# Optimization experiments

Measured on AMD Instinct MI355X. Metric: run time of the kernel, lower is better.

## Reference

```python
import jax, jax.numpy as jnp
from jax import lax
import numpy as np

IMG_W = 384; IMG_H = 384; FEAT = 24; RF = 16
RATIOS = (0.5, 1.0, 2.0); SCALES = (8.0, 16.0, 32.0)
K = 9                      # len(RATIOS) * len(SCALES)
N = FEAT * FEAT * K        # 5184 anchors/proposals
MID = 24; CIN = 512
NMS_THRESH = 0.7; MIN_SIZE = 16.0


def _make_anchors():
    # Faithful port of RPN._get_anchors (vectorized over the grid).
    area = float(RF * RF)
    base = []
    for r in RATIOS:
        cols = np.round(np.sqrt(area / r)); rows = np.round(cols * r)
        x0 = 0.5 * RF - 0.5 * (cols - 1); x1 = 0.5 * RF + 0.5 * (cols - 1)
        y0 = 0.5 * RF - 0.5 * (rows - 1); y1 = 0.5 * RF + 0.5 * (rows - 1)
        aw = x1 - x0 + 1; ah = y1 - y0 + 1
        acx = x0 + 0.5 * (aw - 1); acy = y0 + 0.5 * (ah - 1)
        for s in SCALES:
            nx0 = acx - 0.5 * (aw * s - 1.0); nx1 = acx + 0.5 * (aw * s - 1.0)
            ny0 = acy - 0.5 * (ah * s - 1.0); ny1 = acy + 0.5 * (ah * s - 1.0)
            w = nx1 - nx0 + 1; h = ny1 - ny0 + 1
            base.append([nx0 + 0.5 * (w - 1), ny0 + 0.5 * (h - 1), w, h])
    base = np.asarray(base, np.float32)  # (K,4) as (cx, cy, w, h)
    ii, jj = np.meshgrid(np.arange(FEAT), np.arange(FEAT), indexing='ij')
    g = np.broadcast_to(base, (FEAT, FEAT, K, 4)).copy()  # (H, W, K, 4)
    g[..., 0] += (jj * RF)[:, :, None]
    g[..., 1] += (ii * RF)[:, :, None]
    a = g.reshape(-1, 4)  # matches permute(1,2,0).reshape(-1,4) ordering
    ax0 = a[:, 0] - 0.5 * (a[:, 2] - 1.0); ay0 = a[:, 1] - 0.5 * (a[:, 3] - 1.0)
    ax1 = a[:, 2] + ax0 - 1.0; ay1 = a[:, 3] + ay0 - 1.0
    valid = (ax0 >= 0) & (ay0 >= 0) & (ax1 < IMG_W) & (ay1 < IMG_H)
    return jnp.asarray(a, jnp.float32), jnp.asarray(valid)


def setup_inputs() -> dict:
    key = jax.random.key(0)
    ks = jax.random.split(key, 6)
    anchors, valid_mask = _make_anchors()
    return {
        'x': jax.random.normal(ks[0], (1, CIN, FEAT, FEAT), jnp.float32),
        'labels_class': jax.random.randint(ks[1], (N,), 0, 21, jnp.int32),
        'W_rpn': jax.random.normal(ks[2], (MID, CIN, 3, 3), jnp.float32) * 0.02,
        'b_rpn': jnp.zeros((MID,), jnp.float32),
        'W_cls': jax.random.normal(ks[3], (2 * K, MID), jnp.float32) * 0.05,
        'b_cls': jnp.zeros((2 * K,), jnp.float32),
        'W_reg': jax.random.normal(ks[4], (4 * K, MID), jnp.float32) * 0.01,
        'b_reg': jnp.zeros((4 * K,), jnp.float32),
        'anchors': anchors,
        'valid_mask': valid_mask,
    }


def _forward(x, W_rpn, b_rpn, W_cls, b_cls, W_reg, b_reg, anchors, valid_mask, labels_class):
    # 3x3 conv + relu, then 1x1 cls/reg heads
    h = jax.nn.relu(
        lax.conv_general_dilated(x, W_rpn, (1, 1), ((1, 1), (1, 1)),
                                 dimension_numbers=('NCHW', 'OIHW', 'NCHW'))
        + b_rpn[None, :, None, None])
    cls_out = (jnp.einsum('nchw,oc->nohw', h, W_cls) + b_cls[None, :, None, None])[0]
    cls_out = cls_out.transpose(1, 2, 0).reshape(-1, 2)   # [N,2]
    reg_out = (jnp.einsum('nchw,oc->nohw', h, W_reg) + b_reg[None, :, None, None])[0]
    reg_out = reg_out.transpose(1, 2, 0).reshape(-1, 4)   # [N,4]

    # anchors -> proposals (cx, cy, w, h); computed for all anchors, validity masked below
    ax, ay, aw, ah = anchors[:, 0], anchors[:, 1], anchors[:, 2], anchors[:, 3]
    tx, ty, tw, th = reg_out[:, 0], reg_out[:, 1], reg_out[:, 2], reg_out[:, 3]
    px = ax + aw * tx; py = ay + ah * ty
    pw = aw * jnp.exp(tw); ph = ah * jnp.exp(th)
    proposals = jnp.stack((px, py, pw, ph), axis=1)

    # offset2bbox + clip_boxes
    x0 = px - 0.5 * (pw - 1.0); y0 = py - 0.5 * (ph - 1.0)
    x1 = pw + x0 - 1.0; y1 = ph + y0 - 1.0
    x0 = jnp.clip(x0, 0.0, IMG_W - 1.0); x1 = jnp.clip(x1, 0.0, IMG_W - 1.0)
    y0 = jnp.clip(y0, 0.0, IMG_H - 1.0); y1 = jnp.clip(y1, 0.0, IMG_H - 1.0)
    ws = x1 - x0 + 1.0; hs = y1 - y0 + 1.0

    probs = jax.nn.softmax(cls_out, axis=1)[:, 1]
    validity = valid_mask & (ws >= MIN_SIZE) & (hs >= MIN_SIZE)

    # greedy NMS (padded/masked: invalid boxes get score -1 and are never kept)
    scores = jnp.where(validity, probs, -1.0)
    order = jnp.argsort(-scores)
    bx0, by0, bx1, by1 = x0[order], y0[order], x1[order], y1[order]
    v_sorted = validity[order]
    areas = ws[order] * hs[order]
    iw = jnp.clip(jnp.minimum(bx1[:, None], bx1[None, :]) - jnp.maximum(bx0[:, None], bx0[None, :]) + 1.0, 0.0)
    ih = jnp.clip(jnp.minimum(by1[:, None], by1[None, :]) - jnp.maximum(by0[:, None], by0[None, :]) + 1.0, 0.0)
    inter = iw * ih
    iou = inter / (areas[:, None] + areas[None, :] - inter)  # [N,N]
    idxs = jnp.arange(N)

    def body(sup, xs):
        i, row, v = xs
        keep_i = v & jnp.logical_not(sup[i])
        sup = jnp.where(keep_i, sup | ((row > NMS_THRESH) & (idxs > i)), sup)
        return sup, keep_i

    _, keep_sorted = lax.scan(body, jnp.zeros((N,), bool), (idxs, iou, v_sorted))
    keep = jnp.zeros((N,), bool).at[order].set(keep_sorted)
    keepf = keep.astype(probs.dtype)

    # bbox2offset of kept boxes (padded: suppressed rows zeroed)
    filtered = jnp.stack((x0 + 0.5 * (ws - 1.0), y0 + 0.5 * (hs - 1.0), ws, hs), axis=1) * keepf[:, None]
    probs_kept = probs * keepf
    labels_kept = jnp.where(keep, labels_class, 0)
    return proposals, cls_out, filtered, probs_kept, labels_kept, keep


def reference(x, labels_class, W_rpn, b_rpn, W_cls, b_cls, W_reg, b_reg, anchors, valid_mask):
    return _forward(x, W_rpn, b_rpn, W_cls, b_cls, W_reg, b_reg, anchors, valid_mask, labels_class)
```

## Files before the change

### kernel.cpp

```cpp
#include <hip/hip_runtime.h>
#include <hip/hip_bf16.h>
#include <math.h>

#define NANC   5184
#define NPOS   576
#define CIN    512
#define MIDC   24
#define KANC   9
#define IMGW   384.0f
#define IMGM1  383.0f
#define MINSZ  16.0f
#define THRESH 0.7f

#define OFF_PROP 0
#define OFF_CLS  20736
#define OFF_FILT 31104
#define OFF_PK   51840
#define OFF_LBL  57024
#define OFF_KEEP 62208

#define MCAP 896
#define GCAP 14
#define TOTW (64 * (GCAP*(GCAP+1)/2))

#define WS_XT    0
#define WS_WT    1179648
#define WS_BOX   1622016
#define WS_PROB  1953792
#define WS_KEYS  2036736
#define WS_SIDX  2044928
#define WS_SBOX  2049024
#define WS_MASK  2063360
#define WS_CNT   2117120

__global__ __launch_bounds__(256) void k_prep(const float* __restrict__ x,
                                              const float* __restrict__ W,
                                              float* __restrict__ xt,
                                              float* __restrict__ Wt,
                                              unsigned* cnt) {
    int tid = blockIdx.x * 256 + threadIdx.x;
    if (tid == 0) *cnt = 0;
    const int TOT = CIN * NPOS + MIDC * CIN * 9;
    for (int idx = tid; idx < TOT; idx += gridDim.x * 256) {
        if (idx < CIN * NPOS) {
            int pos = idx >> 9, ic = idx & 511;
            xt[idx] = x[ic * NPOS + pos];
        } else {
            int k = idx - CIN * NPOS;
            int ic = k & 511; int t = k >> 9;
            int oc = t / 9, kk = t % 9;
            Wt[k] = W[(oc * CIN + ic) * 9 + kk];
        }
    }
}

__global__ __launch_bounds__(256) void k_main(
        const float* __restrict__ xt, const float* __restrict__ Wt,
        const float* __restrict__ brpn,
        const float* __restrict__ Wc, const float* __restrict__ bc,
        const float* __restrict__ Wr, const float* __restrict__ br,
        const float* __restrict__ anchors,
        float* __restrict__ out, float4* __restrict__ boxes,
        float* __restrict__ probs, unsigned long long* __restrict__ vkeys,
        unsigned* __restrict__ cnt) {
    const int tid = threadIdx.x;
    const int y = blockIdx.x / 6;
    const int xb = (blockIdx.x % 6) * 4;

    float acc[24][4];
    #pragma unroll
    for (int oc = 0; oc < 24; ++oc)
        #pragma unroll
        for (int p = 0; p < 4; ++p) acc[oc][p] = 0.f;

    for (int half = 0; half < 2; ++half) {
        const int ic = tid + half * 256;
        float xw[3][6];
        #pragma unroll
        for (int r = 0; r < 3; ++r) {
            int yy = y - 1 + r;
            #pragma unroll
            for (int c = 0; c < 6; ++c) {
                int xx = xb - 1 + c;
                bool in = (yy >= 0) & (yy < 24) & (xx >= 0) & (xx < 24);
                xw[r][c] = in ? xt[(yy * 24 + xx) * CIN + ic] : 0.f;
            }
        }
        const float* wp = Wt + ic;
        #pragma unroll
        for (int oc = 0; oc < 24; ++oc) {
            #pragma unroll
            for (int kk = 0; kk < 9; ++kk) {
                const int r = kk / 3, c = kk % 3;
                float wv = wp[(oc * 9 + kk) * CIN];
                #pragma unroll
                for (int p = 0; p < 4; ++p)
                    acc[oc][p] += wv * xw[r][c + p];
            }
        }
    }
    #pragma unroll
    for (int oc = 0; oc < 24; ++oc)
        #pragma unroll
        for (int p = 0; p < 4; ++p) {
            float v = acc[oc][p];
            #pragma unroll
            for (int m = 1; m < 64; m <<= 1) v += __shfl_xor(v, m, 64);
            acc[oc][p] = v;
        }

    __shared__ float red[4][96];
    __shared__ float h_ld[4 * 24];
    __shared__ float cls_ld[4 * 18];
    __shared__ float reg_ld[4 * 36];
    const int wave = tid >> 6, lane = tid & 63;
    if (lane == 0) {
        #pragma unroll
        for (int oc = 0; oc < 24; ++oc)
            #pragma unroll
            for (int p = 0; p < 4; ++p) red[wave][oc * 4 + p] = acc[oc][p];
    }
    __syncthreads();
    if (tid < 96) {
        float s = red[0][tid] + red[1][tid] + red[2][tid] + red[3][tid];
        int oc = tid >> 2, p = tid & 3;
        h_ld[p * 24 + oc] = fmaxf(s + brpn[oc], 0.f);
    }
    __syncthreads();
    if (tid < 216) {
        int p = tid / 54, o = tid % 54;
        const float* hv = h_ld + p * 24;
        if (o < 18) {
            float s = bc[o];
            const float* w = Wc + o * 24;
            #pragma unroll
            for (int c = 0; c < 24; ++c) s += w[c] * hv[c];
            cls_ld[p * 18 + o] = s;
            out[OFF_CLS + (y * 24 + xb + p) * 18 + o] = s;
        } else {
            int o2 = o - 18;
            float s = br[o2];
            const float* w = Wr + o2 * 24;
            #pragma unroll
            for (int c = 0; c < 24; ++c) s += w[c] * hv[c];
            reg_ld[p * 36 + o2] = s;
        }
    }
    __syncthreads();
    if (tid < 36) {
        #pragma clang fp contract(off)
        int p = tid / 9, k = tid % 9;
        int n = (y * 24 + xb + p) * 9 + k;
        float ax = anchors[4 * n], ay = anchors[4 * n + 1];
        float aw = anchors[4 * n + 2], ah = anchors[4 * n + 3];
        float tx = reg_ld[p * 36 + 4 * k],     ty = reg_ld[p * 36 + 4 * k + 1];
        float tw = reg_ld[p * 36 + 4 * k + 2], th = reg_ld[p * 36 + 4 * k + 3];
        float px = ax + aw * tx, py = ay + ah * ty;
        float pw = aw * expf(tw), ph = ah * expf(th);
        out[OFF_PROP + 4 * n]     = px;
        out[OFF_PROP + 4 * n + 1] = py;
        out[OFF_PROP + 4 * n + 2] = pw;
        out[OFF_PROP + 4 * n + 3] = ph;
        float gx0 = ax - 0.5f * (aw - 1.f);
        float gy0 = ay - 0.5f * (ah - 1.f);
        float gx1 = aw + gx0 - 1.f;
        float gy1 = ah + gy0 - 1.f;
        bool geo_ok = (gx0 >= 0.f) & (gy0 >= 0.f) & (gx1 < IMGW) & (gy1 < IMGW);
        float x0 = px - 0.5f * (pw - 1.f);
        float y0 = py - 0.5f * (ph - 1.f);
        float x1 = pw + x0 - 1.f;
        float y1 = ph + y0 - 1.f;
        x0 = fminf(fmaxf(x0, 0.f), IMGM1);
        x1 = fminf(fmaxf(x1, 0.f), IMGM1);
        y0 = fminf(fmaxf(y0, 0.f), IMGM1);
        y1 = fminf(fmaxf(y1, 0.f), IMGM1);
        float wsb = x1 - x0 + 1.f, hsb = y1 - y0 + 1.f;
        float c0 = cls_ld[p * 18 + 2 * k], c1 = cls_ld[p * 18 + 2 * k + 1];
        float mx = fmaxf(c0, c1);
        float e0 = expf(c0 - mx), e1 = expf(c1 - mx);
        float pr = e1 / (e0 + e1);
        boxes[n] = make_float4(x0, y0, x1, y1);
        probs[n] = pr;
        bool valid = geo_ok && (wsb >= MINSZ) && (hsb >= MINSZ);
        if (valid) {
            unsigned pos = atomicAdd(cnt, 1u);
            unsigned u = __float_as_uint(pr);
            unsigned enc = u ^ ((u >> 31) ? 0xFFFFFFFFu : 0x80000000u);
            vkeys[pos] = ((unsigned long long)(~enc) << 32) | (unsigned)n;
        }
    }
}

__global__ __launch_bounds__(512) void k_sort(const unsigned long long* __restrict__ vkeys,
                                              const unsigned* __restrict__ cnt,
                                              int* __restrict__ sidx,
                                              float4* __restrict__ sbox,
                                              const float4* __restrict__ boxes) {
    __shared__ unsigned long long keys[1024];
    const int t = threadIdx.x;
    unsigned Mc = *cnt; unsigned M = Mc < (unsigned)MCAP ? Mc : (unsigned)MCAP;
    for (int i = t; i < 1024; i += 512) keys[i] = (i < (int)M) ? vkeys[i] : ~0ULL;
    __syncthreads();
    for (int k = 2; k <= 1024; k <<= 1) {
        for (int j = k >> 1; j > 0; j >>= 1) {
            int lo = t & (j - 1);
            int i = ((t ^ lo) << 1) | lo;
            int pa = i | j;
            bool up = (i & k) == 0;
            unsigned long long a = keys[i], b = keys[pa];
            if ((a > b) == up) { keys[i] = b; keys[pa] = a; }
            __syncthreads();
        }
    }
    for (int i = t; i < (int)M; i += 512) {
        int n = (int)(keys[i] & 0xFFFFFFFFu);
        sidx[i] = n;
        sbox[i] = boxes[n];
    }
}

__global__ __launch_bounds__(256) void k_mask(const float4* __restrict__ sbox,
                                              const unsigned* __restrict__ cnt,
                                              unsigned long long* __restrict__ mask) {
    __shared__ float4 sb[MCAP];
    const int t = threadIdx.x;
    for (int i = t; i < MCAP; i += 256) sb[i] = sbox[i];
    __syncthreads();
    unsigned Mc = *cnt; unsigned M = Mc < (unsigned)MCAP ? Mc : (unsigned)MCAP;
    int widx = blockIdx.x * 256 + t;
    if (widx >= TOTW) return;
    int g = 0, base = 0;
    while (g < GCAP - 1) {
        int nb = base + 64 * (GCAP - g);
        if (widx < nb) break;
        base = nb; ++g;
    }
    int rem = widx - base;
    int r = rem / (GCAP - g);
    int gw = g + rem % (GCAP - g);
    int i = g * 64 + r;
    if (i >= (int)M) return;
    {
        #pragma clang fp contract(off)
        float4 bi = sb[i];
        float ai = (bi.z - bi.x + 1.f) * (bi.w - bi.y + 1.f);
        unsigned long long w = 0;
        #pragma unroll 4
        for (int b = 0; b < 64; ++b) {
            int j = gw * 64 + b;
            if (j > i) {
                float4 bj = sb[j];
                float iw = fminf(bi.z, bj.z) - fmaxf(bi.x, bj.x) + 1.f;
                float ih = fminf(bi.w, bj.w) - fmaxf(bi.y, bj.y) + 1.f;
                iw = fmaxf(iw, 0.f); ih = fmaxf(ih, 0.f);
                float inter = iw * ih;
                float aj = (bj.z - bj.x + 1.f) * (bj.w - bj.y + 1.f);
                float iou = inter / (ai + aj - inter);
                if (iou > THRESH) w |= 1ULL << b;
            }
        }
        mask[widx] = w;
    }
}

__global__ __launch_bounds__(1024) void k_nms(const unsigned long long* __restrict__ mask_g,
                                              const int* __restrict__ sidx_g,
                                              const unsigned* __restrict__ cnt,
                                              const float4* __restrict__ boxes,
                                              const float* __restrict__ probs,
                                              const int* __restrict__ labels,
                                              float* __restrict__ out) {
    __shared__ unsigned long long mk[TOTW];
    __shared__ int sidx[MCAP];
    __shared__ unsigned long long keepm[81];
    __shared__ unsigned long long keeps[GCAP];
    const int t = threadIdx.x;
    unsigned Mc = *cnt; unsigned M = Mc < (unsigned)MCAP ? Mc : (unsigned)MCAP;
    for (int i = t; i < TOTW; i += 1024) mk[i] = mask_g[i];
    if (t < MCAP) sidx[t] = sidx_g[t];
    if (t < 81) keepm[t] = 0;
    if (t < GCAP) keeps[t] = 0;
    __syncthreads();
    if (t < 64) {
        const int lane = t;
        unsigned long long remv = 0;
        const int ngroups = (int)((M + 63) >> 6);
        for (int g = 0; g < ngroups; ++g) {
            const int rowstride = GCAP - g;
            const int base_g = 64 * (GCAP * g - (g * (g - 1)) / 2);
            unsigned long long diag = mk[base_g + lane * rowstride];
            unsigned dlo = (unsigned)diag, dhi = (unsigned)(diag >> 32);
            unsigned slo = (unsigned)__builtin_amdgcn_readlane((int)(unsigned)remv, g);
            unsigned shi = (unsigned)__builtin_amdgcn_readlane((int)(unsigned)(remv >> 32), g);
            unsigned long long supp = ((unsigned long long)shi << 32) | slo;
            unsigned long long kw = 0;
            int nbits = (int)M - g * 64; if (nbits > 64) nbits = 64;
            for (int r = 0; r < nbits; ++r) {
                if (!((supp >> r) & 1ULL)) {
                    kw |= 1ULL << r;
                    unsigned rlo = (unsigned)__builtin_amdgcn_readlane((int)dlo, r);
                    unsigned rhi = (unsigned)__builtin_amdgcn_readlane((int)dhi, r);
                    supp |= ((unsigned long long)rhi << 32) | rlo;
                }
            }
            if (lane == 0) keeps[g] = kw;
            if (lane > g && lane < GCAP) {
                const unsigned long long* rowp = &mk[base_g + (lane - g)];
                unsigned long long kwi = kw;
                while (kwi) {
                    int r = __ffsll((unsigned long long)kwi) - 1;
                    kwi &= kwi - 1;
                    remv |= rowp[r * rowstride];
                }
            }
        }
    }
    __syncthreads();
    if (t < (int)M) {
        if ((keeps[t >> 6] >> (t & 63)) & 1ULL) {
            int n = sidx[t];
            atomicOr(&keepm[n >> 6], 1ULL << (n & 63));
        }
    }
    __syncthreads();
    for (int n = t; n < NANC; n += 1024) {
        unsigned long long kb = (keepm[n >> 6] >> (n & 63)) & 1ULL;
        float kf = kb ? 1.f : 0.f;
        float4 b = boxes[n];
        float wsb = b.z - b.x + 1.f, hsb = b.w - b.y + 1.f;
        out[OFF_FILT + 4 * n]     = (b.x + 0.5f * (wsb - 1.f)) * kf;
        out[OFF_FILT + 4 * n + 1] = (b.y + 0.5f * (hsb - 1.f)) * kf;
        out[OFF_FILT + 4 * n + 2] = wsb * kf;
        out[OFF_FILT + 4 * n + 3] = hsb * kf;
        out[OFF_PK + n]  = probs[n] * kf;
        out[OFF_LBL + n] = kb ? (float)labels[n] : 0.f;
        out[OFF_KEEP + n] = kf;
    }
}

extern "C" void kernel_launch(void* const* d_in, const int* in_sizes, int n_in,
                              void* d_out, int out_size, void* d_ws, size_t ws_size,
                              hipStream_t stream) {
    const float* x        = (const float*)d_in[0];
    const int*   labels   = (const int*)d_in[1];
    const float* Wrpn     = (const float*)d_in[2];
    const float* brpn     = (const float*)d_in[3];
    const float* Wcls     = (const float*)d_in[4];
    const float* bcls     = (const float*)d_in[5];
    const float* Wreg     = (const float*)d_in[6];
    const float* breg     = (const float*)d_in[7];
    const float* anchors  = (const float*)d_in[8];
    float* out = (float*)d_out;
    char* ws = (char*)d_ws;

    float*  xt    = (float*)(ws + WS_XT);
    float*  Wt    = (float*)(ws + WS_WT);
    float4* boxes = (float4*)(ws + WS_BOX);
    float*  probs = (float*)(ws + WS_PROB);
    unsigned long long* vkeys = (unsigned long long*)(ws + WS_KEYS);
    int*    sidx  = (int*)(ws + WS_SIDX);
    float4* sbox  = (float4*)(ws + WS_SBOX);
    unsigned long long* mask = (unsigned long long*)(ws + WS_MASK);
    unsigned* cnt = (unsigned*)(ws + WS_CNT);

    k_prep<<<1584, 256, 0, stream>>>(x, Wrpn, xt, Wt, cnt);
    k_main<<<144, 256, 0, stream>>>(xt, Wt, brpn, Wcls, bcls, Wreg, breg,
                                    anchors, out, boxes, probs, vkeys, cnt);
    k_sort<<<1, 512, 0, stream>>>(vkeys, cnt, sidx, sbox, boxes);
    k_mask<<<27, 256, 0, stream>>>(sbox, cnt, mask);
    k_nms<<<1, 1024, 0, stream>>>(mask, sidx, cnt, boxes, probs, labels, out);
}
```

Measured before the change: 171.8 us.

## Parallelize NMS cross-group suppression across waves and skip empty diagonal rows

The serial greedy scan inside each 64-box group now iterates only over rows whose diagonal mask is nonzero, found with a ballot. Rows with no in-group overlaps stay kept unless an earlier box suppresses them. Propagating kept rows to later groups moves from a serial loop on a few lanes to one wave per later group, with each wave OR-reducing via shuffles and writing to a shared suppression word. This trades the single-wave serial propagation for two block-wide barriers per group.

```diff
diff --git a/kernel.cpp b/kernel.cpp
--- a/kernel.cpp
+++ b/kernel.cpp
@@ -274,48 +274,53 @@
     __shared__ int sidx[MCAP];
     __shared__ unsigned long long keepm[81];
     __shared__ unsigned long long keeps[GCAP];
+    __shared__ unsigned long long suppw[GCAP];
     const int t = threadIdx.x;
     unsigned Mc = *cnt; unsigned M = Mc < (unsigned)MCAP ? Mc : (unsigned)MCAP;
     for (int i = t; i < TOTW; i += 1024) mk[i] = mask_g[i];
     if (t < MCAP) sidx[t] = sidx_g[t];
     if (t < 81) keepm[t] = 0;
-    if (t < GCAP) keeps[t] = 0;
-    __syncthreads();
-    if (t < 64) {
-        const int lane = t;
-        unsigned long long remv = 0;
-        const int ngroups = (int)((M + 63) >> 6);
-        for (int g = 0; g < ngroups; ++g) {
-            const int rowstride = GCAP - g;
-            const int base_g = 64 * (GCAP * g - (g * (g - 1)) / 2);
+    if (t < GCAP) { keeps[t] = 0; suppw[t] = 0; }
+    __syncthreads();
+    const int wid = t >> 6, lane = t & 63;
+    const int ngroups = (int)((M + 63) >> 6);
+    for (int g = 0; g < ngroups; ++g) {
+        const int rowstride = GCAP - g;
+        const int base_g = 64 * (GCAP * g - (g * (g - 1)) / 2);
+        int nbits = (int)M - g * 64; if (nbits > 64) nbits = 64;
+        unsigned long long vmaskbits = (nbits < 64) ? ((1ULL << nbits) - 1ULL) : ~0ULL;
+        if (wid == 0) {
             unsigned long long diag = mk[base_g + lane * rowstride];
             unsigned dlo = (unsigned)diag, dhi = (unsigned)(diag >> 32);
-            unsigned slo = (unsigned)__builtin_amdgcn_readlane((int)(unsigned)remv, g);
-            unsigned shi = (unsigned)__builtin_amdgcn_readlane((int)(unsigned)(remv >> 32), g);
-            unsigned long long supp = ((unsigned long long)shi << 32) | slo;
-            unsigned long long kw = 0;
-            int nbits = (int)M - g * 64; if (nbits > 64) nbits = 64;
-            for (int r = 0; r < nbits; ++r) {
+            unsigned long long supp = suppw[g];
+            unsigned long long nz = __ballot(diag != 0ULL) & vmaskbits;
+            while (nz) {
+                int r = __ffsll(nz) - 1;
+                nz &= nz - 1;
                 if (!((supp >> r) & 1ULL)) {
-                    kw |= 1ULL << r;
                     unsigned rlo = (unsigned)__builtin_amdgcn_readlane((int)dlo, r);
                     unsigned rhi = (unsigned)__builtin_amdgcn_readlane((int)dhi, r);
                     supp |= ((unsigned long long)rhi << 32) | rlo;
                 }
             }
-            if (lane == 0) keeps[g] = kw;
-            if (lane > g && lane < GCAP) {
-                const unsigned long long* rowp = &mk[base_g + (lane - g)];
-                unsigned long long kwi = kw;
-                while (kwi) {
-                    int r = __ffsll((unsigned long long)kwi) - 1;
-                    kwi &= kwi - 1;
-                    remv |= rowp[r * rowstride];
-                }
-            }
-        }
-    }
-    __syncthreads();
+            if (lane == 0) keeps[g] = ~supp & vmaskbits;
+        }
+        __syncthreads();
+        if (wid > g && wid < GCAP) {
+            unsigned long long kw = keeps[g];
+            unsigned long long v = ((kw >> lane) & 1ULL)
+                ? mk[base_g + lane * rowstride + (wid - g)] : 0ULL;
+            unsigned vlo = (unsigned)v, vhi = (unsigned)(v >> 32);
+            #pragma unroll
+            for (int m = 1; m < 64; m <<= 1) {
+                vlo |= __shfl_xor(vlo, m, 64);
+                vhi |= __shfl_xor(vhi, m, 64);
+            }
+            if (lane == 0)
+                suppw[wid] |= ((unsigned long long)vhi << 32) | vlo;
+        }
+        __syncthreads();
+    }
     if (t < (int)M) {
         if ((keeps[t >> 6] >> (t & 63)) & 1ULL) {
             int n = sidx[t];
```

Measured after the change: 139.3 us. 1.23x faster.
